# Performance work log

Measured on AMD Instinct MI355X. Metric: run time of the kernel, lower is better.

Reference implementation:

```python
import jax, jax.numpy as jnp
import numpy as np

B, N, C_IN, C_OUT, M = 32, 4096, 128, 128, 256


def setup_inputs() -> dict:
    key = jax.random.key(0)
    k1, k2, k3, k4 = jax.random.split(key, 4)
    x = jax.random.normal(k1, (B, N, C_IN), dtype=jnp.float32)
    # Lowest-M eigenvectors of a graph Laplacian are orthonormal columns [N, M];
    # build an equivalent orthonormal basis via QR of a random matrix.
    U, _ = jnp.linalg.qr(jax.random.normal(k2, (N, M), dtype=jnp.float32))
    # complex spectral weights ~ 0.02 * randn (cfloat) split into real/imag parts
    W_real = jax.random.normal(k3, (C_IN, C_OUT, M), dtype=jnp.float32) * 0.02
    W_imag = jax.random.normal(k4, (C_IN, C_OUT, M), dtype=jnp.float32) * 0.02
    return {"x": x, "eigenvectors": U, "W_real": W_real, "W_imag": W_imag}


def reference(x, eigenvectors, W_real, W_imag):
    # Graph Fourier transform: project node features onto spectral modes.
    # x_spec[b, m, c] = sum_n U[n, m] * x[b, n, c]
    x_spec = jnp.einsum('nm,bnc->bmc', eigenvectors, x)  # [B, M, C_in], real
    # Per-mode complex channel mixing, fused into one batched einsum.
    # Original takes .real of (x_spec * W); since x_spec is real,
    # Re(x_spec @ W) = x_spec @ Re(W), so W_imag does not affect the output.
    out_spec_real = jnp.einsum('bmc,com->bmo', x_spec, W_real)  # [B, M, C_out]
    # Inverse graph Fourier transform back to node space.
    return jnp.einsum('nm,bmo->bno', eigenvectors, out_spec_real)  # [B, N, C_out]
```

## Files before the change

### kernel.cpp

```cpp
#include <hip/hip_runtime.h>
#include <hip/hip_bf16.h>

#define BB 32
#define NN 4096
#define CI 128
#define CO 128
#define MM 256
#define KS 8

typedef __hip_bfloat16 bf16;
typedef __attribute__((ext_vector_type(8))) short bf16x8;
typedef __attribute__((ext_vector_type(4))) float f32x4;

__device__ inline void gl_lds16(const void* g, void* l) {
    __builtin_amdgcn_global_load_lds(
        (const __attribute__((address_space(1))) void*)g,
        (__attribute__((address_space(3))) void*)l, 16, 0, 0);
}

__global__ __launch_bounds__(256) void k_prep(const float* __restrict__ U,
                                              const float* __restrict__ W,
                                              bf16* __restrict__ Un,
                                              bf16* __restrict__ Ut,
                                              bf16* __restrict__ Wt) {
    const int blk = blockIdx.x;
    const int t = threadIdx.x;
    __shared__ float tile[64][65];
    if (blk < 256) {
        const int n0 = (blk & 63) * 64;
        const int m0 = (blk >> 6) * 64;
        #pragma unroll
        for (int i = 0; i < 16; ++i) {
            int lin = t + i * 256;
            int r = lin >> 6, c = lin & 63;
            float v = U[(n0 + r) * MM + m0 + c];
            tile[r][c] = v;
            Un[(n0 + r) * MM + m0 + c] = __float2bfloat16(v);
        }
        __syncthreads();
        #pragma unroll
        for (int pass = 0; pass < 2; ++pass) {
            int no = t & 7;
            int m  = (t >> 3) + pass * 32;
            bf16 tmp[8];
            #pragma unroll
            for (int j = 0; j < 8; ++j) tmp[j] = __float2bfloat16(tile[no * 8 + j][m]);
            *(bf16x8*)&Ut[(long)(m0 + m) * NN + n0 + no * 8] = *(bf16x8*)tmp;
        }
    } else {
        const int q  = blk - 256;
        const int c  = q >> 3;
        const int m0 = (q & 3) * 64;
        const int o0 = ((q >> 2) & 1) * 64;
        #pragma unroll
        for (int pass = 0; pass < 4; ++pass) {
            int r  = (t >> 4) + pass * 16;
            int m4 = (t & 15) * 4;
            float4 v = *(const float4*)&W[((long)c * CO + o0 + r) * MM + m0 + m4];
            tile[r][m4 + 0] = v.x; tile[r][m4 + 1] = v.y;
            tile[r][m4 + 2] = v.z; tile[r][m4 + 3] = v.w;
        }
        __syncthreads();
        #pragma unroll
        for (int pass = 0; pass < 2; ++pass) {
            int oo = t & 7;
            int m  = (t >> 3) + pass * 32;
            bf16 tmp[8];
            #pragma unroll
            for (int j = 0; j < 8; ++j) tmp[j] = __float2bfloat16(tile[oo * 8 + j][m]);
            *(bf16x8*)&Wt[((long)(m0 + m) * CI + c) * CO + o0 + oo * 8] = *(bf16x8*)tmp;
        }
    }
}

__global__ __launch_bounds__(256) void k_gemm1f(const bf16* __restrict__ Ut,
                                                const float* __restrict__ x,
                                                bf16* __restrict__ part) {
    const int bx = blockIdx.x;
    const int ks = bx & 7;
    const int mt = (bx >> 3) & 1;
    const int b  = bx >> 4;
    const int m0 = mt * 128;
    __shared__ __align__(16) bf16  As[2][128 * 32];
    __shared__ __align__(16) bf16  Bs[2][128 * 32];
    __shared__ __align__(16) float Xf[2][32 * 128];
    const int t    = threadIdx.x;
    const int lane = t & 63;
    const int wave = t >> 6;
    const int wm   = wave >> 1, wn = wave & 1;
    const int fr   = lane & 15;
    const int kg   = (lane >> 4) * 8;
    f32x4 acc[4][4] = {};
    const long xrow  = (long)b * NN;
    const int  kbase = ks * 512;

    auto STAGE = [&](int buf, int kt) {
        const int k0 = kbase + kt * 32;
        #pragma unroll
        for (int i = 0; i < 2; ++i) {
            int lin = t + i * 256;
            int r = lin >> 2, kk = (lin & 3) * 8;
            gl_lds16(&Ut[(long)(m0 + r) * NN + k0 + kk], &As[buf][lin * 8]);
        }
        #pragma unroll
        for (int i = 0; i < 4; ++i) {
            int lin = t + i * 256;
            int r = lin >> 5, c4 = (lin & 31) * 4;
            gl_lds16(&x[(xrow + k0 + r) * CI + c4], &Xf[buf][lin * 4]);
        }
    };

    STAGE(0, 0);
    __syncthreads();
    for (int kt = 0; kt < 16; ++kt) {
        const int cur = kt & 1;
        {
            const int c = t & 127;
            #pragma unroll
            for (int pass = 0; pass < 2; ++pass) {
                int no = (t >> 7) + pass * 2;
                bf16 tmp[8];
                #pragma unroll
                for (int j = 0; j < 8; ++j)
                    tmp[j] = __float2bfloat16(Xf[cur][(no * 8 + j) * 128 + c]);
                *(bf16x8*)&Bs[cur][c * 32 + no * 8] = *(bf16x8*)tmp;
            }
        }
        __syncthreads();
        if (kt + 1 < 16) STAGE(cur ^ 1, kt + 1);
        bf16x8 a[4], bfr[4];
        #pragma unroll
        for (int i = 0; i < 4; ++i)
            a[i] = *(const bf16x8*)&As[cur][(wm * 64 + i * 16 + fr) * 32 + kg];
        #pragma unroll
        for (int j = 0; j < 4; ++j)
            bfr[j] = *(const bf16x8*)&Bs[cur][(wn * 64 + j * 16 + fr) * 32 + kg];
        #pragma unroll
        for (int i = 0; i < 4; ++i)
            #pragma unroll
            for (int j = 0; j < 4; ++j)
                acc[i][j] = __builtin_amdgcn_mfma_f32_16x16x32_bf16(a[i], bfr[j], acc[i][j], 0, 0, 0);
        __syncthreads();
    }
    const int quad = (lane >> 4) * 4;
    const long pbase = ((long)ks * BB + b) * MM * CI;
    #pragma unroll
    for (int i = 0; i < 4; ++i) {
        #pragma unroll
        for (int j = 0; j < 4; ++j) {
            int mg = m0 + wm * 64 + i * 16 + quad;
            int cg = wn * 64 + j * 16 + fr;
            #pragma unroll
            for (int r = 0; r < 4; ++r)
                part[pbase + (long)(mg + r) * CI + cg] = __float2bfloat16(acc[i][j][r]);
        }
    }
}

__global__ __launch_bounds__(256) void k_mix(const bf16* __restrict__ part,
                                             const bf16* __restrict__ Wt,
                                             bf16* __restrict__ osT) {
    const int blk = blockIdx.x;
    const int m   = (blk & 7) * 32 + (blk >> 3);
    __shared__ bf16  Wl[CI][CO];
    __shared__ float xl[CI][36];
    const int t = threadIdx.x;
    const long wb = (long)m * CI * CO;
    #pragma unroll
    for (int i = 0; i < 8; ++i) {
        int ch = t + i * 256;
        int c = ch >> 4, og = (ch & 15) * 8;
        *(bf16x8*)&Wl[c][og] = *(const bf16x8*)&Wt[wb + (long)c * CO + og];
    }
    #pragma unroll
    for (int i = 0; i < 2; ++i) {
        int ch = t + i * 256;
        int b = ch >> 4, c8 = (ch & 15) * 8;
        float s[8] = {};
        #pragma unroll
        for (int ks = 0; ks < KS; ++ks) {
            bf16x8 v = *(const bf16x8*)&part[(((long)ks * BB + b) * MM + m) * CI + c8];
            #pragma unroll
            for (int j = 0; j < 8; ++j) s[j] += __bfloat162float(((const bf16*)&v)[j]);
        }
        #pragma unroll
        for (int j = 0; j < 8; ++j) xl[c8 + j][b] = s[j];
    }
    __syncthreads();
    const int o  = t & 127;
    const int bh = t >> 7;
    float acc[16] = {};
    for (int c = 0; c < CI; ++c) {
        float w = __bfloat162float(Wl[c][o]);
        #pragma unroll
        for (int j = 0; j < 16; ++j)
            acc[j] += xl[c][bh * 16 + j] * w;
    }
    #pragma unroll
    for (int j = 0; j < 16; ++j)
        osT[((long)(bh * 16 + j) * CO + o) * MM + m] = __float2bfloat16(acc[j]);
}

__global__ __launch_bounds__(256) void k_gemm3(const bf16* __restrict__ Un,
                                               const bf16* __restrict__ osT,
                                               float* __restrict__ out) {
    const int n0 = blockIdx.x * 128;
    const int b  = blockIdx.y;
    __shared__ __align__(16) bf16 As[128 * 32];
    __shared__ __align__(16) bf16 Bs[128 * 32];
    const int t    = threadIdx.x;
    const int lane = t & 63;
    const int wave = t >> 6;
    const int wm   = wave >> 1, wn = wave & 1;
    const int fr   = lane & 15;
    const int kg   = (lane >> 4) * 8;
    f32x4 acc[4][4] = {};
    const long bbase = (long)b * CO * MM;
    for (int kt = 0; kt < MM / 32; ++kt) {
        const int k0 = kt * 32;
        #pragma unroll
        for (int i = 0; i < 2; ++i) {
            int lin = t + i * 256;
            int r = lin >> 2, kk = (lin & 3) * 8;
            gl_lds16(&Un[(long)(n0 + r) * MM + k0 + kk], &As[lin * 8]);
            gl_lds16(&osT[bbase + (long)r * MM + k0 + kk], &Bs[lin * 8]);
        }
        __syncthreads();
        bf16x8 a[4], bfr[4];
        #pragma unroll
        for (int i = 0; i < 4; ++i)
            a[i] = *(const bf16x8*)&As[(wm * 64 + i * 16 + fr) * 32 + kg];
        #pragma unroll
        for (int j = 0; j < 4; ++j)
            bfr[j] = *(const bf16x8*)&Bs[(wn * 64 + j * 16 + fr) * 32 + kg];
        #pragma unroll
        for (int i = 0; i < 4; ++i)
            #pragma unroll
            for (int j = 0; j < 4; ++j)
                acc[i][j] = __builtin_amdgcn_mfma_f32_16x16x32_bf16(a[i], bfr[j], acc[i][j], 0, 0, 0);
        __syncthreads();
    }
    const int quad = (lane >> 4) * 4;
    #pragma unroll
    for (int i = 0; i < 4; ++i) {
        #pragma unroll
        for (int j = 0; j < 4; ++j) {
            int ng = n0 + wm * 64 + i * 16 + quad;
            int og = wn * 64 + j * 16 + fr;
            #pragma unroll
            for (int r = 0; r < 4; ++r)
                out[((long)b * NN + ng + r) * CO + og] = acc[i][j][r];
        }
    }
}

extern "C" void kernel_launch(void* const* d_in, const int* in_sizes, int n_in,
                              void* d_out, int out_size, void* d_ws, size_t ws_size,
                              hipStream_t stream) {
    const float* x  = (const float*)d_in[0];
    const float* U  = (const float*)d_in[1];
    const float* Wr = (const float*)d_in[2];
    float* out = (float*)d_out;

    char* p = (char*)d_ws;
    bf16* part = (bf16*)p;  p += (size_t)KS * BB * MM * CI * 2;
    bf16* Ut   = (bf16*)p;  p += (size_t)MM * NN * 2;
    bf16* Un   = (bf16*)p;  p += (size_t)NN * MM * 2;
    bf16* osT  = (bf16*)p;  p += (size_t)BB * CO * MM * 2;
    bf16* Wt   = (bf16*)p;  p += (size_t)MM * CI * CO * 2;

    k_prep  <<<dim3(1280), 256, 0, stream>>>(U, Wr, Un, Ut, Wt);
    k_gemm1f<<<dim3(KS * 2 * BB), 256, 0, stream>>>(Ut, x, part);
    k_mix   <<<dim3(256), 256, 0, stream>>>(part, Wt, osT);
    k_gemm3 <<<dim3(NN / 128, BB), 256, 0, stream>>>(Un, osT, out);
}
```

Measured before the change: 182.9 us.

## Enlarge gemm3 tile to 256 rows reusing B fragments; vectorize mix LDS reads

k_gemm3 now computes 256 node rows per block instead of 128, so each loaded osT tile and its B fragments are reused across two A tiles. The grid is flattened to 512 blocks with a launch-bounds occupancy hint of 2. Each thread now holds twice as many accumulators, which raises register pressure. Separately, k_mix pads its xl shared array to 40 floats per row and reads it as float4 vectors to cut LDS instruction count.

```diff
diff --git a/kernel.cpp b/kernel.cpp
--- a/kernel.cpp
+++ b/kernel.cpp
@@ -163,7 +163,7 @@
     const int blk = blockIdx.x;
     const int m   = (blk & 7) * 32 + (blk >> 3);
     __shared__ bf16  Wl[CI][CO];
-    __shared__ float xl[CI][36];
+    __shared__ float xl[CI][40];
     const int t = threadIdx.x;
     const long wb = (long)m * CI * CO;
     #pragma unroll
@@ -192,21 +192,25 @@
     float acc[16] = {};
     for (int c = 0; c < CI; ++c) {
         float w = __bfloat162float(Wl[c][o]);
-        #pragma unroll
-        for (int j = 0; j < 16; ++j)
-            acc[j] += xl[c][bh * 16 + j] * w;
+        const float4* xr = (const float4*)&xl[c][bh * 16];
+        float4 v0 = xr[0], v1 = xr[1], v2 = xr[2], v3 = xr[3];
+        acc[0]  += v0.x * w; acc[1]  += v0.y * w; acc[2]  += v0.z * w; acc[3]  += v0.w * w;
+        acc[4]  += v1.x * w; acc[5]  += v1.y * w; acc[6]  += v1.z * w; acc[7]  += v1.w * w;
+        acc[8]  += v2.x * w; acc[9]  += v2.y * w; acc[10] += v2.z * w; acc[11] += v2.w * w;
+        acc[12] += v3.x * w; acc[13] += v3.y * w; acc[14] += v3.z * w; acc[15] += v3.w * w;
     }
     #pragma unroll
     for (int j = 0; j < 16; ++j)
         osT[((long)(bh * 16 + j) * CO + o) * MM + m] = __float2bfloat16(acc[j]);
 }
 
-__global__ __launch_bounds__(256) void k_gemm3(const bf16* __restrict__ Un,
-                                               const bf16* __restrict__ osT,
-                                               float* __restrict__ out) {
-    const int n0 = blockIdx.x * 128;
-    const int b  = blockIdx.y;
-    __shared__ __align__(16) bf16 As[128 * 32];
+__global__ __launch_bounds__(256, 2) void k_gemm3(const bf16* __restrict__ Un,
+                                                  const bf16* __restrict__ osT,
+                                                  float* __restrict__ out) {
+    const int bx = blockIdx.x;
+    const int np = bx & 15;
+    const int b  = bx >> 4;
+    __shared__ __align__(16) bf16 As[2][128 * 32];
     __shared__ __align__(16) bf16 Bs[128 * 32];
     const int t    = threadIdx.x;
     const int lane = t & 63;
@@ -214,42 +218,51 @@
     const int wm   = wave >> 1, wn = wave & 1;
     const int fr   = lane & 15;
     const int kg   = (lane >> 4) * 8;
-    f32x4 acc[4][4] = {};
+    f32x4 acc[2][4][4] = {};
     const long bbase = (long)b * CO * MM;
+    const int  nb    = np * 256;
     for (int kt = 0; kt < MM / 32; ++kt) {
         const int k0 = kt * 32;
         #pragma unroll
         for (int i = 0; i < 2; ++i) {
             int lin = t + i * 256;
             int r = lin >> 2, kk = (lin & 3) * 8;
-            gl_lds16(&Un[(long)(n0 + r) * MM + k0 + kk], &As[lin * 8]);
-            gl_lds16(&osT[bbase + (long)r * MM + k0 + kk], &Bs[lin * 8]);
-        }
-        __syncthreads();
-        bf16x8 a[4], bfr[4];
-        #pragma unroll
-        for (int i = 0; i < 4; ++i)
-            a[i] = *(const bf16x8*)&As[(wm * 64 + i * 16 + fr) * 32 + kg];
+            gl_lds16(&Un[(long)(nb + r) * MM + k0 + kk],       &As[0][lin * 8]);
+            gl_lds16(&Un[(long)(nb + 128 + r) * MM + k0 + kk], &As[1][lin * 8]);
+            gl_lds16(&osT[bbase + (long)r * MM + k0 + kk],     &Bs[lin * 8]);
+        }
+        __syncthreads();
+        bf16x8 bfr[4];
         #pragma unroll
         for (int j = 0; j < 4; ++j)
             bfr[j] = *(const bf16x8*)&Bs[(wn * 64 + j * 16 + fr) * 32 + kg];
         #pragma unroll
-        for (int i = 0; i < 4; ++i)
-            #pragma unroll
-            for (int j = 0; j < 4; ++j)
-                acc[i][j] = __builtin_amdgcn_mfma_f32_16x16x32_bf16(a[i], bfr[j], acc[i][j], 0, 0, 0);
+        for (int rr = 0; rr < 2; ++rr) {
+            bf16x8 a[4];
+            #pragma unroll
+            for (int i = 0; i < 4; ++i)
+                a[i] = *(const bf16x8*)&As[rr][(wm * 64 + i * 16 + fr) * 32 + kg];
+            #pragma unroll
+            for (int i = 0; i < 4; ++i)
+                #pragma unroll
+                for (int j = 0; j < 4; ++j)
+                    acc[rr][i][j] = __builtin_amdgcn_mfma_f32_16x16x32_bf16(a[i], bfr[j], acc[rr][i][j], 0, 0, 0);
+        }
         __syncthreads();
     }
     const int quad = (lane >> 4) * 4;
     #pragma unroll
-    for (int i = 0; i < 4; ++i) {
-        #pragma unroll
-        for (int j = 0; j < 4; ++j) {
-            int ng = n0 + wm * 64 + i * 16 + quad;
-            int og = wn * 64 + j * 16 + fr;
-            #pragma unroll
-            for (int r = 0; r < 4; ++r)
-                out[((long)b * NN + ng + r) * CO + og] = acc[i][j][r];
+    for (int rr = 0; rr < 2; ++rr) {
+        #pragma unroll
+        for (int i = 0; i < 4; ++i) {
+            #pragma unroll
+            for (int j = 0; j < 4; ++j) {
+                int ng = nb + rr * 128 + wm * 64 + i * 16 + quad;
+                int og = wn * 64 + j * 16 + fr;
+                #pragma unroll
+                for (int r = 0; r < 4; ++r)
+                    out[((long)b * NN + ng + r) * CO + og] = acc[rr][i][j][r];
+            }
         }
     }
 }
@@ -272,5 +285,5 @@
     k_prep  <<<dim3(1280), 256, 0, stream>>>(U, Wr, Un, Ut, Wt);
     k_gemm1f<<<dim3(KS * 2 * BB), 256, 0, stream>>>(Ut, x, part);
     k_mix   <<<dim3(256), 256, 0, stream>>>(part, Wt, osT);
-    k_gemm3 <<<dim3(NN / 128, BB), 256, 0, stream>>>(Un, osT, out);
-}
+    k_gemm3 <<<dim3(512), 256, 0, stream>>>(Un, osT, out);
+}
```

After: 184.4 us. Within noise of the previous version (+0.9%).

## Triple-buffer gemm1 loads with manual vmcnt waits and vectorize mix LDS reads

Applied to the files above, without the earlier changes.

The first GEMM moves from a double-buffered stage to a three-deep ring buffer for U and x tiles. It issues loads two and three iterations ahead and replaces __syncthreads with explicit s_waitcnt vmcnt and raw barriers, so global loads overlap more compute. The bf16 B tile becomes a single buffer. The mix kernel pads the x tile row to 40 floats so reads can use float4 vector LDS loads. Hand-counted vmcnt values risk races if the compiler reorders or the load count changes, and the extra buffers increase LDS use, which may lower occupancy.

```diff
diff --git a/kernel.cpp b/kernel.cpp
--- a/kernel.cpp
+++ b/kernel.cpp
@@ -17,6 +17,9 @@
         (const __attribute__((address_space(1))) void*)g,
         (__attribute__((address_space(3))) void*)l, 16, 0, 0);
 }
+
+#define CFENCE() asm volatile("" ::: "memory")
+#define BAR()    __builtin_amdgcn_s_barrier()
 
 __global__ __launch_bounds__(256) void k_prep(const float* __restrict__ U,
                                               const float* __restrict__ W,
@@ -81,9 +84,9 @@
     const int mt = (bx >> 3) & 1;
     const int b  = bx >> 4;
     const int m0 = mt * 128;
-    __shared__ __align__(16) bf16  As[2][128 * 32];
-    __shared__ __align__(16) bf16  Bs[2][128 * 32];
-    __shared__ __align__(16) float Xf[2][32 * 128];
+    __shared__ __align__(16) bf16  As[3][128 * 32];
+    __shared__ __align__(16) bf16  Bs[128 * 32];
+    __shared__ __align__(16) float Xf[3][32 * 128];
     const int t    = threadIdx.x;
     const int lane = t & 63;
     const int wave = t >> 6;
@@ -93,8 +96,9 @@
     f32x4 acc[4][4] = {};
     const long xrow  = (long)b * NN;
     const int  kbase = ks * 512;
-
-    auto STAGE = [&](int buf, int kt) {
+    const int  NT    = 16;
+
+    auto STAGE_A = [&](int buf, int kt) {
         const int k0 = kbase + kt * 32;
         #pragma unroll
         for (int i = 0; i < 2; ++i) {
@@ -102,6 +106,9 @@
             int r = lin >> 2, kk = (lin & 3) * 8;
             gl_lds16(&Ut[(long)(m0 + r) * NN + k0 + kk], &As[buf][lin * 8]);
         }
+    };
+    auto STAGE_X = [&](int buf, int kt) {
+        const int k0 = kbase + kt * 32;
         #pragma unroll
         for (int i = 0; i < 4; ++i) {
             int lin = t + i * 256;
@@ -110,10 +117,14 @@
         }
     };
 
-    STAGE(0, 0);
-    __syncthreads();
-    for (int kt = 0; kt < 16; ++kt) {
-        const int cur = kt & 1;
+    STAGE_X(0, 0);
+    STAGE_A(0, 0); STAGE_X(1, 1);
+    STAGE_A(1, 1); STAGE_X(2, 2);
+    asm volatile("s_waitcnt vmcnt(10)" ::: "memory");
+    BAR(); CFENCE();
+
+    for (int kt = 0; kt < NT; ++kt) {
+        const int xb = kt % 3;
         {
             const int c = t & 127;
             #pragma unroll
@@ -122,25 +133,31 @@
                 bf16 tmp[8];
                 #pragma unroll
                 for (int j = 0; j < 8; ++j)
-                    tmp[j] = __float2bfloat16(Xf[cur][(no * 8 + j) * 128 + c]);
-                *(bf16x8*)&Bs[cur][c * 32 + no * 8] = *(bf16x8*)tmp;
+                    tmp[j] = __float2bfloat16(Xf[xb][(no * 8 + j) * 128 + c]);
+                *(bf16x8*)&Bs[c * 32 + no * 8] = *(bf16x8*)tmp;
             }
         }
-        __syncthreads();
-        if (kt + 1 < 16) STAGE(cur ^ 1, kt + 1);
+        asm volatile("s_waitcnt lgkmcnt(0)" ::: "memory");
+        BAR(); CFENCE();
         bf16x8 a[4], bfr[4];
         #pragma unroll
         for (int i = 0; i < 4; ++i)
-            a[i] = *(const bf16x8*)&As[cur][(wm * 64 + i * 16 + fr) * 32 + kg];
+            a[i] = *(const bf16x8*)&As[xb][(wm * 64 + i * 16 + fr) * 32 + kg];
         #pragma unroll
         for (int j = 0; j < 4; ++j)
-            bfr[j] = *(const bf16x8*)&Bs[cur][(wn * 64 + j * 16 + fr) * 32 + kg];
+            bfr[j] = *(const bf16x8*)&Bs[(wn * 64 + j * 16 + fr) * 32 + kg];
         #pragma unroll
         for (int i = 0; i < 4; ++i)
             #pragma unroll
             for (int j = 0; j < 4; ++j)
                 acc[i][j] = __builtin_amdgcn_mfma_f32_16x16x32_bf16(a[i], bfr[j], acc[i][j], 0, 0, 0);
-        __syncthreads();
+        CFENCE();
+        if (kt + 2 < NT) STAGE_A((kt + 2) % 3, kt + 2);
+        if (kt + 3 < NT) STAGE_X((kt + 3) % 3, kt + 3);
+        if (kt + 3 < NT)      asm volatile("s_waitcnt vmcnt(10)" ::: "memory");
+        else if (kt + 2 < NT) asm volatile("s_waitcnt vmcnt(6)"  ::: "memory");
+        else                  asm volatile("s_waitcnt vmcnt(0)"  ::: "memory");
+        BAR(); CFENCE();
     }
     const int quad = (lane >> 4) * 4;
     const long pbase = ((long)ks * BB + b) * MM * CI;
@@ -163,7 +180,7 @@
     const int blk = blockIdx.x;
     const int m   = (blk & 7) * 32 + (blk >> 3);
     __shared__ bf16  Wl[CI][CO];
-    __shared__ float xl[CI][36];
+    __shared__ float xl[CI][40];
     const int t = threadIdx.x;
     const long wb = (long)m * CI * CO;
     #pragma unroll
@@ -192,9 +209,12 @@
     float acc[16] = {};
     for (int c = 0; c < CI; ++c) {
         float w = __bfloat162float(Wl[c][o]);
-        #pragma unroll
-        for (int j = 0; j < 16; ++j)
-            acc[j] += xl[c][bh * 16 + j] * w;
+        const float4* xr = (const float4*)&xl[c][bh * 16];
+        float4 v0 = xr[0], v1 = xr[1], v2 = xr[2], v3 = xr[3];
+        acc[0]  += v0.x * w; acc[1]  += v0.y * w; acc[2]  += v0.z * w; acc[3]  += v0.w * w;
+        acc[4]  += v1.x * w; acc[5]  += v1.y * w; acc[6]  += v1.z * w; acc[7]  += v1.w * w;
+        acc[8]  += v2.x * w; acc[9]  += v2.y * w; acc[10] += v2.z * w; acc[11] += v2.w * w;
+        acc[12] += v3.x * w; acc[13] += v3.y * w; acc[14] += v3.z * w; acc[15] += v3.w * w;
     }
     #pragma unroll
     for (int j = 0; j < 16; ++j)
```

Result: no change. 184.4 us (+0.8%).
